# Kernel tuning notes

Measured on AMD Instinct MI355X. Metric: run time of the kernel, lower is better.

## Reference

```python
import jax, jax.numpy as jnp
import numpy as np

S = 4  # HMM states
# allowed transitions among the 4 recurrent states (plus self-loops);
# the (0,4) edge targets a terminal state outside the recurrent block and is omitted
_allow = np.zeros((S, S), dtype=bool)
for i, j in [(0, 0), (1, 1), (2, 2), (3, 3), (0, 1), (1, 2), (2, 3), (0, 2), (1, 3)]:
    _allow[i, j] = True
MASK = jnp.asarray(_allow)
NEG = -1e9


def setup_inputs() -> dict:
    key = jax.random.key(0)
    k0, k1, k2, k3, k4 = jax.random.split(key, 5)
    return {
        "x": jax.random.normal(k0, (256, 4096, 26), dtype=jnp.float32),
        "emit_logits": jax.random.normal(k1, (S, 26), dtype=jnp.float32) * 0.3,
        "trans_logits": jax.random.normal(k2, (S, S), dtype=jnp.float32) * 0.3,
        "init_logits": jax.random.normal(k3, (S,), dtype=jnp.float32) * 0.3,
        "w_out": jax.random.normal(k4, (1, S, 5), dtype=jnp.float32) * 0.3,
    }


def _posterior(x, emit_logits, trans_logits, init_logits):
    # x: [B,T,A] logits -> softmax over alphabet (as in call())
    p = jax.nn.softmax(x, axis=-1)                       # [B,T,A]
    Bmat = jax.nn.softmax(emit_logits, axis=-1)          # [S,A] emission distributions
    # expected emission likelihood per state, in log space
    log_emit = jnp.log(jnp.einsum('bta,sa->bts', p, Bmat) + 1e-16)  # [B,T,S]

    neg = jnp.asarray(NEG, x.dtype)
    logA = jax.nn.log_softmax(jnp.where(MASK, trans_logits, neg), axis=-1)
    logA = jnp.where(MASK, logA, neg)                    # [S,S]
    log_pi = jax.nn.log_softmax(init_logits)             # [S]

    le = jnp.moveaxis(log_emit, 1, 0)                    # [T,B,S]
    T = le.shape[0]

    # forward recursion: alpha_t = e_t + LSE_prev(alpha_{t-1} + logA)
    a0 = log_pi[None, :] + le[0]                         # [B,S]
    def fstep(carry, e):
        nc = e + jax.nn.logsumexp(carry[:, :, None] + logA[None], axis=1)
        return nc, nc
    _, alphas = jax.lax.scan(fstep, a0, le[1:])
    alphas = jnp.concatenate([a0[None], alphas], axis=0)  # [T,B,S]

    # backward recursion: beta_t = LSE_next(logA + e_{t+1} + beta_{t+1})
    bT = jnp.zeros_like(a0)
    def bstep(carry, e_next):
        nc = jax.nn.logsumexp(logA[None] + (e_next + carry)[:, None, :], axis=2)
        return nc, nc
    _, betas = jax.lax.scan(bstep, bT, le[1:], reverse=True)
    betas = jnp.concatenate([betas, bT[None]], axis=0)    # [T,B,S]

    gamma = jax.nn.softmax(alphas + betas, axis=-1)       # posterior [T,B,S]
    return jnp.moveaxis(gamma, 0, 1)[:, :, None, :]       # [B,T,1,S]


def reference(x, emit_logits, trans_logits, init_logits, w_out):
    gamma = _posterior(x, emit_logits, trans_logits, init_logits)  # [B,T,1,S]
    return jnp.einsum('bthd,hdo->bto', gamma, w_out)               # [B,T,5]
```

## Files before the change

### kernel.cpp

```cpp
#include <hip/hip_runtime.h>

#define TDIM 4096
#define BDIM 256
#define ADIM 26
#define SDIM 4
#define NEGF -1e30f
#define LOG2E 1.44269504088896340736f

__device__ __forceinline__ float ex2(float x) { return __builtin_amdgcn_exp2f(x); }
__device__ __forceinline__ float lg2(float x) { return __builtin_amdgcn_logf(x); }

__device__ __forceinline__ float l2se2(float a, float b) {
    float mx = fmaxf(a, b), mn = fminf(a, b);
    return mx + lg2(1.f + ex2(mn - mx));
}
__device__ __forceinline__ float l2se3(float a, float b, float c) {
    float mx = fmaxf(fmaxf(a, b), c);
    float md = __builtin_amdgcn_fmed3f(a, b, c);
    float mn = fminf(fminf(a, b), c);
    return mx + lg2(1.f + ex2(md - mx) + ex2(mn - mx));
}
__device__ __forceinline__ float l2se4(float a, float b, float c, float d) {
    float h1 = fmaxf(a, b), l1 = fminf(a, b);
    float h2 = fmaxf(c, d), l2 = fminf(c, d);
    float mx = fmaxf(h1, h2), s2 = fminf(h1, h2);
    return mx + lg2(1.f + ex2(s2 - mx) + ex2(l1 - mx) + ex2(l2 - mx));
}

struct TransA { float A00, A01, A02, A11, A12, A13, A22, A23, A33; };

__device__ __forceinline__ TransA make_transA(const float* __restrict__ trans) {
    TransA A;
    {
        float l0 = trans[0], l1 = trans[1], l2 = trans[2];
        float m = fmaxf(fmaxf(l0, l1), l2);
        float lz = m + __logf(__expf(l0 - m) + __expf(l1 - m) + __expf(l2 - m));
        A.A00 = (l0 - lz) * LOG2E; A.A01 = (l1 - lz) * LOG2E; A.A02 = (l2 - lz) * LOG2E;
    }
    {
        float l1 = trans[5], l2 = trans[6], l3 = trans[7];
        float m = fmaxf(fmaxf(l1, l2), l3);
        float lz = m + __logf(__expf(l1 - m) + __expf(l2 - m) + __expf(l3 - m));
        A.A11 = (l1 - lz) * LOG2E; A.A12 = (l2 - lz) * LOG2E; A.A13 = (l3 - lz) * LOG2E;
    }
    {
        float l2 = trans[10], l3 = trans[11];
        float m = fmaxf(l2, l3);
        float lz = m + __logf(__expf(l2 - m) + __expf(l3 - m));
        A.A22 = (l2 - lz) * LOG2E; A.A23 = (l3 - lz) * LOG2E;
    }
    A.A33 = 0.f;
    return A;
}

struct UT { float m00, m01, m02, m03, m11, m12, m13, m22, m23, m33; };

__device__ __forceinline__ void fstep(UT& M, const TransA& A, float4 e) {
    float n00 = M.m00 + A.A00 + e.x;
    float n01 = l2se2(M.m00 + A.A01, M.m01 + A.A11) + e.y;
    float n02 = l2se3(M.m00 + A.A02, M.m01 + A.A12, M.m02 + A.A22) + e.z;
    float n03 = l2se3(M.m01 + A.A13, M.m02 + A.A23, M.m03) + e.w;
    float n11 = M.m11 + A.A11 + e.y;
    float n12 = l2se2(M.m11 + A.A12, M.m12 + A.A22) + e.z;
    float n13 = l2se3(M.m11 + A.A13, M.m12 + A.A23, M.m13) + e.w;
    float n22 = M.m22 + A.A22 + e.z;
    float n23 = l2se2(M.m22 + A.A23, M.m23) + e.w;
    float n33 = M.m33 + e.w;
    M.m00 = n00; M.m01 = n01; M.m02 = n02; M.m03 = n03;
    M.m11 = n11; M.m12 = n12; M.m13 = n13; M.m22 = n22; M.m23 = n23; M.m33 = n33;
}

__device__ __forceinline__ UT ut_compose(const UT& A, const UT& B) {
    UT C;
    C.m00 = A.m00 + B.m00;
    C.m01 = l2se2(A.m00 + B.m01, A.m01 + B.m11);
    C.m02 = l2se3(A.m00 + B.m02, A.m01 + B.m12, A.m02 + B.m22);
    C.m03 = l2se4(A.m00 + B.m03, A.m01 + B.m13, A.m02 + B.m23, A.m03 + B.m33);
    C.m11 = A.m11 + B.m11;
    C.m12 = l2se2(A.m11 + B.m12, A.m12 + B.m22);
    C.m13 = l2se3(A.m11 + B.m13, A.m12 + B.m23, A.m13 + B.m33);
    C.m22 = A.m22 + B.m22;
    C.m23 = l2se2(A.m22 + B.m23, A.m23 + B.m33);
    C.m33 = A.m33 + B.m33;
    return C;
}

__device__ __forceinline__ void ut_renorm(UT& M) {
    float m1 = fmaxf(fmaxf(M.m00, M.m01), fmaxf(M.m02, M.m03));
    float m2 = fmaxf(fmaxf(M.m11, M.m12), fmaxf(M.m13, M.m22));
    float m3 = fmaxf(M.m23, M.m33);
    float mx = fmaxf(fmaxf(m1, m2), m3);
    M.m00 -= mx; M.m01 -= mx; M.m02 -= mx; M.m03 -= mx;
    M.m11 -= mx; M.m12 -= mx; M.m13 -= mx; M.m22 -= mx; M.m23 -= mx; M.m33 -= mx;
}

__device__ __forceinline__ void ut_store11(float* p, const UT& M) {
    p[0] = M.m00; p[1] = M.m01; p[2] = M.m02; p[3] = M.m03;
    p[4] = M.m11; p[5] = M.m12; p[6] = M.m13;
    p[7] = M.m22; p[8] = M.m23; p[9] = M.m33;
}
__device__ __forceinline__ UT ut_load11(const float* p) {
    UT M;
    M.m00 = p[0]; M.m01 = p[1]; M.m02 = p[2]; M.m03 = p[3];
    M.m11 = p[4]; M.m12 = p[5]; M.m13 = p[6];
    M.m22 = p[7]; M.m23 = p[8]; M.m33 = p[9];
    return M;
}

__device__ __forceinline__ void vecmat(float& v0, float& v1, float& v2, float& v3,
                                       const float* m) {
    float n0 = v0 + m[0];
    float n1 = l2se2(v0 + m[1], v1 + m[4]);
    float n2 = l2se3(v0 + m[2], v1 + m[5], v2 + m[7]);
    float n3 = l2se4(v0 + m[3], v1 + m[6], v2 + m[8], v3 + m[9]);
    float mm = fmaxf(fmaxf(n0, n1), fmaxf(n2, n3));
    v0 = n0 - mm; v1 = n1 - mm; v2 = n2 - mm; v3 = n3 - mm;
}
__device__ __forceinline__ void matvec(const float* m,
                                       float& u0, float& u1, float& u2, float& u3) {
    float n0 = l2se4(m[0] + u0, m[1] + u1, m[2] + u2, m[3] + u3);
    float n1 = l2se3(m[4] + u1, m[5] + u2, m[6] + u3);
    float n2 = l2se2(m[7] + u2, m[8] + u3);
    float n3 = m[9] + u3;
    float mm = fmaxf(fmaxf(n0, n1), fmaxf(n2, n3));
    u0 = n0 - mm; u1 = n1 - mm; u2 = n2 - mm; u3 = n3 - mm;
}

#define ASTEP(E) do { \
    float4 _e = (E); \
    float n0_ = a0 + A.A00; \
    float n1_ = l2se2(a0 + A.A01, a1 + A.A11); \
    float n2_ = l2se3(a0 + A.A02, a1 + A.A12, a2 + A.A22); \
    float n3_ = l2se3(a1 + A.A13, a2 + A.A23, a3); \
    a0 = n0_ + _e.x; a1 = n1_ + _e.y; a2 = n2_ + _e.z; a3 = n3_ + _e.w; \
    float mm_ = fmaxf(fmaxf(a0, a1), fmaxf(a2, a3)); \
    a0 -= mm_; a1 -= mm_; a2 -= mm_; a3 -= mm_; \
} while (0)

#define BSTEP(E) do { \
    float4 _e = (E); \
    float f0_ = _e.x + b0, f1_ = _e.y + b1, f2_ = _e.z + b2, f3_ = _e.w + b3; \
    float n0_ = l2se3(A.A00 + f0_, A.A01 + f1_, A.A02 + f2_); \
    float n1_ = l2se3(A.A11 + f1_, A.A12 + f2_, A.A13 + f3_); \
    float n2_ = l2se2(A.A22 + f2_, A.A23 + f3_); \
    float n3_ = f3_; \
    float bm_ = fmaxf(fmaxf(n0_, n1_), fmaxf(n2_, n3_)); \
    b0 = n0_ - bm_; b1 = n1_ - bm_; b2 = n2_ - bm_; b3 = n3_ - bm_; \
} while (0)

#define GEMIT(AV, Q) do { \
    float g0_ = (AV).x + b0, g1_ = (AV).y + b1, g2_ = (AV).z + b2, g3_ = (AV).w + b3; \
    float gm_ = fmaxf(fmaxf(g0_, g1_), fmaxf(g2_, g3_)); \
    float q0_ = ex2(g0_ - gm_), q1_ = ex2(g1_ - gm_); \
    float q2_ = ex2(g2_ - gm_), q3_ = ex2(g3_ - gm_); \
    float inv_ = 1.f / (q0_ + q1_ + q2_ + q3_); \
    q0_ *= inv_; q1_ *= inv_; q2_ *= inv_; q3_ *= inv_; \
    vals[(Q)*5 + 0] = fmaf(q0_, wv[0][0], fmaf(q1_, wv[1][0], fmaf(q2_, wv[2][0], q3_ * wv[3][0]))); \
    vals[(Q)*5 + 1] = fmaf(q0_, wv[0][1], fmaf(q1_, wv[1][1], fmaf(q2_, wv[2][1], q3_ * wv[3][1]))); \
    vals[(Q)*5 + 2] = fmaf(q0_, wv[0][2], fmaf(q1_, wv[1][2], fmaf(q2_, wv[2][2], q3_ * wv[3][2]))); \
    vals[(Q)*5 + 3] = fmaf(q0_, wv[0][3], fmaf(q1_, wv[1][3], fmaf(q2_, wv[2][3], q3_ * wv[3][3]))); \
    vals[(Q)*5 + 4] = fmaf(q0_, wv[0][4], fmaf(q1_, wv[1][4], fmaf(q2_, wv[2][4], q3_ * wv[3][4]))); \
} while (0)

#define RDLE(T) sle[(((T) & 15) * 257) + ((T) >> 4)]

#define L0F 0
#define L0B 2816
#define L1F 5632
#define L1B 7040
#define L2F 8448
#define L2B 9152
#define L3F 9856
#define L3B 10208
#define SF  10560
#define SB  10688

__global__ __launch_bounds__(512, 1)
void fused_kernel(const float* __restrict__ x, const float* __restrict__ emit,
                  const float* __restrict__ trans, const float* __restrict__ initl,
                  const float* __restrict__ w, float* __restrict__ out) {
    __shared__ float4 sle[16 * 257];
    __shared__ float4 uni[4096];
    __shared__ float Bmat[SDIM][ADIM];

    float* U = reinterpret_cast<float*>(uni);
    float4* abuf = uni;
    float4* bbuf = uni + 2048;

    const int tid = threadIdx.x;
    const int bidb = blockIdx.x;

    if (tid < SDIM) {
        float m = -1e30f;
        #pragma unroll
        for (int a = 0; a < ADIM; ++a) m = fmaxf(m, emit[tid * ADIM + a]);
        float tmp[ADIM];
        float z = 0.f;
        #pragma unroll
        for (int a = 0; a < ADIM; ++a) {
            float e = __expf(emit[tid * ADIM + a] - m);
            tmp[a] = e; z += e;
        }
        float inv = 1.f / z;
        #pragma unroll
        for (int a = 0; a < ADIM; ++a) Bmat[tid][a] = tmp[a] * inv;
    }
    TransA A = make_transA(trans);
    __syncthreads();

    {
        const float4* xbase = reinterpret_cast<const float4*>(x) + (size_t)bidb * 2048 * 13;
        #pragma unroll 1
        for (int i = 0; i < 4; ++i) {
            const float4* xp = xbase + ((size_t)(i * 512 + tid)) * 13;
            float4 buf[13];
            #pragma unroll
            for (int q = 0; q < 13; ++q) buf[q] = xp[q];

            float d00 = 0.f, d01 = 0.f, d02 = 0.f, d03 = 0.f;
            float d10 = 0.f, d11 = 0.f, d12 = 0.f, d13 = 0.f;
            #pragma unroll
            for (int q = 0; q < 13; ++q) {
                float4 u = buf[q];
                #pragma unroll
                for (int j = 0; j < 4; ++j) {
                    const int e = q * 4 + j;
                    float val = (j == 0) ? u.x : (j == 1) ? u.y : (j == 2) ? u.z : u.w;
                    float ev = ex2(val * LOG2E);
                    if (e < ADIM) {
                        d00 = fmaf(ev, Bmat[0][e], d00); d01 = fmaf(ev, Bmat[1][e], d01);
                        d02 = fmaf(ev, Bmat[2][e], d02); d03 = fmaf(ev, Bmat[3][e], d03);
                    } else {
                        const int a = e - ADIM;
                        d10 = fmaf(ev, Bmat[0][a], d10); d11 = fmaf(ev, Bmat[1][a], d11);
                        d12 = fmaf(ev, Bmat[2][a], d12); d13 = fmaf(ev, Bmat[3][a], d13);
                    }
                }
            }
            float4 r0, r1;
            r0.x = lg2(d00); r0.y = lg2(d01); r0.z = lg2(d02); r0.w = lg2(d03);
            r1.x = lg2(d10); r1.y = lg2(d11); r1.z = lg2(d12); r1.w = lg2(d13);
            int t = (i * 512 + tid) << 1;
            RDLE(t) = r0;
            RDLE(t + 1) = r1;
        }
    }
    __syncthreads();

    const int c = tid & 255;
    const int t0 = c * 16;
    const bool isB = tid >= 256;

    {
        UT M;
        if (!isB) {
            float4 e0 = RDLE(t0);
            if (c == 0) {
                M.m00 = e0.x; M.m11 = e0.y; M.m22 = e0.z; M.m33 = e0.w;
                M.m01 = NEGF; M.m02 = NEGF; M.m03 = NEGF; M.m12 = NEGF; M.m13 = NEGF; M.m23 = NEGF;
            } else {
                M.m00 = A.A00 + e0.x; M.m01 = A.A01 + e0.y; M.m02 = A.A02 + e0.z; M.m03 = NEGF;
                M.m11 = A.A11 + e0.y; M.m12 = A.A12 + e0.z; M.m13 = A.A13 + e0.w;
                M.m22 = A.A22 + e0.z; M.m23 = A.A23 + e0.w; M.m33 = e0.w;
            }
            #pragma unroll 1
            for (int k = 1; k < 16; ++k) fstep(M, A, RDLE(t0 + k));
            ut_renorm(M);
            ut_store11(U + L0F + c * 11, M);
        } else {
            M.m00 = 0.f; M.m11 = 0.f; M.m22 = 0.f; M.m33 = 0.f;
            M.m01 = NEGF; M.m02 = NEGF; M.m03 = NEGF; M.m12 = NEGF; M.m13 = NEGF; M.m23 = NEGF;
            int nst = (c == 255) ? 15 : 16;
            #pragma unroll 1
            for (int k = 0; k < nst; ++k) fstep(M, A, RDLE(t0 + 1 + k));
            ut_renorm(M);
            ut_store11(U + L0B + c * 11, M);
        }
    }
    __syncthreads();

    if (tid < 256) {
        int dir = tid >> 7;
        int i = tid & 127;
        const float* src = U + (dir ? L0B : L0F);
        float* dst = U + (dir ? L1B : L1F);
        UT P = ut_compose(ut_load11(src + (2 * i) * 11), ut_load11(src + (2 * i + 1) * 11));
        ut_renorm(P);
        ut_store11(dst + i * 11, P);
    }
    __syncthreads();

    if (tid < 128) {
        int dir = tid >> 6;
        int i = tid & 63;
        const float* src = U + (dir ? L1B : L1F);
        float* dst = U + (dir ? L2B : L2F);
        UT P = ut_compose(ut_load11(src + (2 * i) * 11), ut_load11(src + (2 * i + 1) * 11));
        ut_renorm(P);
        ut_store11(dst + i * 11, P);
    }
    __syncthreads();

    if (tid < 64) {
        int dir = tid >> 5;
        int i = tid & 31;
        const float* src = U + (dir ? L2B : L2F);
        float* dst = U + (dir ? L3B : L3F);
        UT P = ut_compose(ut_load11(src + (2 * i) * 11), ut_load11(src + (2 * i + 1) * 11));
        ut_renorm(P);
        ut_store11(dst + i * 11, P);
    }
    __syncthreads();

    if (tid == 0) {
        float i0 = initl[0], i1 = initl[1], i2 = initl[2], i3 = initl[3];
        float m = fmaxf(fmaxf(i0, i1), fmaxf(i2, i3));
        float lz = m + __logf(__expf(i0 - m) + __expf(i1 - m) + __expf(i2 - m) + __expf(i3 - m));
        float v0 = (i0 - lz) * LOG2E, v1 = (i1 - lz) * LOG2E;
        float v2 = (i2 - lz) * LOG2E, v3 = (i3 - lz) * LOG2E;
        #pragma unroll 1
        for (int g = 0; g < 32; ++g) {
            U[SF + g * 4 + 0] = v0; U[SF + g * 4 + 1] = v1;
            U[SF + g * 4 + 2] = v2; U[SF + g * 4 + 3] = v3;
            vecmat(v0, v1, v2, v3, U + L3F + g * 11);
        }
    } else if (tid == 64) {
        float u0 = 0.f, u1 = 0.f, u2 = 0.f, u3 = 0.f;
        #pragma unroll 1
        for (int g = 31; g >= 0; --g) {
            U[SB + g * 4 + 0] = u0; U[SB + g * 4 + 1] = u1;
            U[SB + g * 4 + 2] = u2; U[SB + g * 4 + 3] = u3;
            matvec(U + L3B + g * 11, u0, u1, u2, u3);
        }
    }
    __syncthreads();

    float fa0, fa1, fa2, fa3;
    float fb0, fb1, fb2, fb3;
    {
        int g = c >> 3;
        if (!isB) {
            fa0 = U[SF + g * 4 + 0]; fa1 = U[SF + g * 4 + 1];
            fa2 = U[SF + g * 4 + 2]; fa3 = U[SF + g * 4 + 3];
            if (c & 4) vecmat(fa0, fa1, fa2, fa3, U + L2F + (2 * g) * 11);
            if (c & 2) vecmat(fa0, fa1, fa2, fa3, U + L1F + ((c >> 2) * 2) * 11);
            if (c & 1) vecmat(fa0, fa1, fa2, fa3, U + L0F + (c - 1) * 11);
        } else {
            fb0 = U[SB + g * 4 + 0]; fb1 = U[SB + g * 4 + 1];
            fb2 = U[SB + g * 4 + 2]; fb3 = U[SB + g * 4 + 3];
            if (!(c & 4)) matvec(U + L2B + (2 * g + 1) * 11, fb0, fb1, fb2, fb3);
            if (!(c & 2)) matvec(U + L1B + ((c >> 2) * 2 + 1) * 11, fb0, fb1, fb2, fb3);
            if (!(c & 1)) matvec(U + L0B + (c + 1) * 11, fb0, fb1, fb2, fb3);
        }
    }
    __syncthreads();

    float wv[SDIM][5];
    #pragma unroll
    for (int s = 0; s < SDIM; ++s)
        #pragma unroll
        for (int o = 0; o < 5; ++o) wv[s][o] = w[s * 5 + o];

    float* opb = out + (size_t)bidb * TDIM * 5;
    float vals[20];

    if (!isB) {
        float a0 = fa0, a1 = fa1, a2 = fa2, a3 = fa3;
        if (c == 0) {
            float4 e = RDLE(0);
            a0 += e.x; a1 += e.y; a2 += e.z; a3 += e.w;
            float mm = fmaxf(fmaxf(a0, a1), fmaxf(a2, a3));
            a0 -= mm; a1 -= mm; a2 -= mm; a3 -= mm;
        } else {
            ASTEP(RDLE(t0));
        }
        abuf[0 * 256 + c] = make_float4(a0, a1, a2, a3);
        #pragma unroll 1
        for (int k = 1; k < 8; ++k) {
            ASTEP(RDLE(t0 + k));
            abuf[k * 256 + c] = make_float4(a0, a1, a2, a3);
        }
        __syncthreads();
        float b0, b1, b2, b3;
        #pragma unroll 1
        for (int g2 = 0; g2 < 2; ++g2) {
            #pragma unroll
            for (int q = 0; q < 4; ++q) {
                int k = 8 + g2 * 4 + q;
                ASTEP(RDLE(t0 + k));
                float4 bv = bbuf[(k - 8) * 256 + c];
                b0 = bv.x; b1 = bv.y; b2 = bv.z; b3 = bv.w;
                float4 av = make_float4(a0, a1, a2, a3);
                GEMIT(av, q);
            }
            float4* vo = reinterpret_cast<float4*>(opb + (size_t)(t0 + 8 + g2 * 4) * 5);
            vo[0] = make_float4(vals[0],  vals[1],  vals[2],  vals[3]);
            vo[1] = make_float4(vals[4],  vals[5],  vals[6],  vals[7]);
            vo[2] = make_float4(vals[8],  vals[9],  vals[10], vals[11]);
            vo[3] = make_float4(vals[12], vals[13], vals[14], vals[15]);
            vo[4] = make_float4(vals[16], vals[17], vals[18], vals[19]);
        }
    } else {
        float b0 = fb0, b1 = fb1, b2 = fb2, b3 = fb3;
        bool lastc = (c == 255);
        #pragma unroll 1
        for (int k = 15; k >= 8; --k) {
            if (!(lastc && k == 15)) BSTEP(RDLE(t0 + 1 + k));
            bbuf[(k - 8) * 256 + c] = make_float4(b0, b1, b2, b3);
        }
        __syncthreads();
        #pragma unroll 1
        for (int g2 = 1; g2 >= 0; --g2) {
            #pragma unroll
            for (int q = 3; q >= 0; --q) {
                int k = g2 * 4 + q;
                BSTEP(RDLE(t0 + 1 + k));
                float4 av = abuf[k * 256 + c];
                GEMIT(av, q);
            }
            float4* vo = reinterpret_cast<float4*>(opb + (size_t)(t0 + g2 * 4) * 5);
            vo[0] = make_float4(vals[0],  vals[1],  vals[2],  vals[3]);
            vo[1] = make_float4(vals[4],  vals[5],  vals[6],  vals[7]);
            vo[2] = make_float4(vals[8],  vals[9],  vals[10], vals[11]);
            vo[3] = make_float4(vals[12], vals[13], vals[14], vals[15]);
            vo[4] = make_float4(vals[16], vals[17], vals[18], vals[19]);
        }
    }
}

extern "C" void kernel_launch(void* const* d_in, const int* in_sizes, int n_in,
                              void* d_out, int out_size, void* d_ws, size_t ws_size,
                              hipStream_t stream) {
    const float* x     = (const float*)d_in[0];
    const float* emit  = (const float*)d_in[1];
    const float* trans = (const float*)d_in[2];
    const float* initl = (const float*)d_in[3];
    const float* w     = (const float*)d_in[4];
    float* out = (float*)d_out;

    hipLaunchKernelGGL(fused_kernel, dim3(BDIM), dim3(512), 0, stream,
                       x, emit, trans, initl, w, out);
}
```

Measured before the change: 47.50 us.

## Double threads per block and halve chunk length in parallel-scan HMM

Raises the block from 512 to 1024 threads so each forward/backward thread handles 8 timesteps instead of 16. An extra level is added to the composition tree of transition matrices, and the shared-memory layouts and offsets are resized to match. The aim is to shorten the serial per-thread chain and hide more latency with more waves per CU. In exchange there is one more tree level and barrier, more shared memory, and more registers per thread count limit under launch_bounds 1024.

```diff
diff --git a/kernel.cpp b/kernel.cpp
--- a/kernel.cpp
+++ b/kernel.cpp
@@ -162,25 +162,27 @@
     vals[(Q)*5 + 4] = fmaf(q0_, wv[0][4], fmaf(q1_, wv[1][4], fmaf(q2_, wv[2][4], q3_ * wv[3][4]))); \
 } while (0)
 
-#define RDLE(T) sle[(((T) & 15) * 257) + ((T) >> 4)]
+#define RDLE(T) sle[(((T) & 7) * 513) + ((T) >> 3)]
 
 #define L0F 0
-#define L0B 2816
-#define L1F 5632
-#define L1B 7040
-#define L2F 8448
-#define L2B 9152
-#define L3F 9856
-#define L3B 10208
-#define SF  10560
-#define SB  10688
-
-__global__ __launch_bounds__(512, 1)
+#define L0B 5632
+#define L1F 11264
+#define L1B 14080
+#define L2F 16896
+#define L2B 18304
+#define L3F 19712
+#define L3B 20416
+#define L4F 21120
+#define L4B 21472
+#define SF  21824
+#define SB  21952
+
+__global__ __launch_bounds__(1024, 1)
 void fused_kernel(const float* __restrict__ x, const float* __restrict__ emit,
                   const float* __restrict__ trans, const float* __restrict__ initl,
                   const float* __restrict__ w, float* __restrict__ out) {
-    __shared__ float4 sle[16 * 257];
-    __shared__ float4 uni[4096];
+    __shared__ float4 sle[8 * 513];
+    __shared__ float4 uni[5520];
     __shared__ float Bmat[SDIM][ADIM];
 
     float* U = reinterpret_cast<float*>(uni);
@@ -211,8 +213,8 @@
     {
         const float4* xbase = reinterpret_cast<const float4*>(x) + (size_t)bidb * 2048 * 13;
         #pragma unroll 1
-        for (int i = 0; i < 4; ++i) {
-            const float4* xp = xbase + ((size_t)(i * 512 + tid)) * 13;
+        for (int i = 0; i < 2; ++i) {
+            const float4* xp = xbase + ((size_t)(i * 1024 + tid)) * 13;
             float4 buf[13];
             #pragma unroll
             for (int q = 0; q < 13; ++q) buf[q] = xp[q];
@@ -240,16 +242,16 @@
             float4 r0, r1;
             r0.x = lg2(d00); r0.y = lg2(d01); r0.z = lg2(d02); r0.w = lg2(d03);
             r1.x = lg2(d10); r1.y = lg2(d11); r1.z = lg2(d12); r1.w = lg2(d13);
-            int t = (i * 512 + tid) << 1;
+            int t = (i * 1024 + tid) << 1;
             RDLE(t) = r0;
             RDLE(t + 1) = r1;
         }
     }
     __syncthreads();
 
-    const int c = tid & 255;
-    const int t0 = c * 16;
-    const bool isB = tid >= 256;
+    const int c = tid & 511;
+    const int t0 = c * 8;
+    const bool isB = tid >= 512;
 
     {
         UT M;
@@ -264,13 +266,13 @@
                 M.m22 = A.A22 + e0.z; M.m23 = A.A23 + e0.w; M.m33 = e0.w;
             }
             #pragma unroll 1
-            for (int k = 1; k < 16; ++k) fstep(M, A, RDLE(t0 + k));
+            for (int k = 1; k < 8; ++k) fstep(M, A, RDLE(t0 + k));
             ut_renorm(M);
             ut_store11(U + L0F + c * 11, M);
         } else {
             M.m00 = 0.f; M.m11 = 0.f; M.m22 = 0.f; M.m33 = 0.f;
             M.m01 = NEGF; M.m02 = NEGF; M.m03 = NEGF; M.m12 = NEGF; M.m13 = NEGF; M.m23 = NEGF;
-            int nst = (c == 255) ? 15 : 16;
+            int nst = (c == 511) ? 7 : 8;
             #pragma unroll 1
             for (int k = 0; k < nst; ++k) fstep(M, A, RDLE(t0 + 1 + k));
             ut_renorm(M);
@@ -279,9 +281,8 @@
     }
     __syncthreads();
 
-    if (tid < 256) {
-        int dir = tid >> 7;
-        int i = tid & 127;
+    if (tid < 512) {
+        int dir = tid >> 8, i = tid & 255;
         const float* src = U + (dir ? L0B : L0F);
         float* dst = U + (dir ? L1B : L1F);
         UT P = ut_compose(ut_load11(src + (2 * i) * 11), ut_load11(src + (2 * i + 1) * 11));
@@ -290,9 +291,8 @@
     }
     __syncthreads();
 
-    if (tid < 128) {
-        int dir = tid >> 6;
-        int i = tid & 63;
+    if (tid < 256) {
+        int dir = tid >> 7, i = tid & 127;
         const float* src = U + (dir ? L1B : L1F);
         float* dst = U + (dir ? L2B : L2F);
         UT P = ut_compose(ut_load11(src + (2 * i) * 11), ut_load11(src + (2 * i + 1) * 11));
@@ -301,11 +301,20 @@
     }
     __syncthreads();
 
-    if (tid < 64) {
-        int dir = tid >> 5;
-        int i = tid & 31;
+    if (tid < 128) {
+        int dir = tid >> 6, i = tid & 63;
         const float* src = U + (dir ? L2B : L2F);
         float* dst = U + (dir ? L3B : L3F);
+        UT P = ut_compose(ut_load11(src + (2 * i) * 11), ut_load11(src + (2 * i + 1) * 11));
+        ut_renorm(P);
+        ut_store11(dst + i * 11, P);
+    }
+    __syncthreads();
+
+    if (tid < 64) {
+        int dir = tid >> 5, i = tid & 31;
+        const float* src = U + (dir ? L3B : L3F);
+        float* dst = U + (dir ? L4B : L4F);
         UT P = ut_compose(ut_load11(src + (2 * i) * 11), ut_load11(src + (2 * i + 1) * 11));
         ut_renorm(P);
         ut_store11(dst + i * 11, P);
@@ -322,7 +331,7 @@
         for (int g = 0; g < 32; ++g) {
             U[SF + g * 4 + 0] = v0; U[SF + g * 4 + 1] = v1;
             U[SF + g * 4 + 2] = v2; U[SF + g * 4 + 3] = v3;
-            vecmat(v0, v1, v2, v3, U + L3F + g * 11);
+            vecmat(v0, v1, v2, v3, U + L4F + g * 11);
         }
     } else if (tid == 64) {
         float u0 = 0.f, u1 = 0.f, u2 = 0.f, u3 = 0.f;
@@ -330,7 +339,7 @@
         for (int g = 31; g >= 0; --g) {
             U[SB + g * 4 + 0] = u0; U[SB + g * 4 + 1] = u1;
             U[SB + g * 4 + 2] = u2; U[SB + g * 4 + 3] = u3;
-            matvec(U + L3B + g * 11, u0, u1, u2, u3);
+            matvec(U + L4B + g * 11, u0, u1, u2, u3);
         }
     }
     __syncthreads();
@@ -338,17 +347,19 @@
     float fa0, fa1, fa2, fa3;
     float fb0, fb1, fb2, fb3;
     {
-        int g = c >> 3;
+        int g = c >> 4;
         if (!isB) {
             fa0 = U[SF + g * 4 + 0]; fa1 = U[SF + g * 4 + 1];
             fa2 = U[SF + g * 4 + 2]; fa3 = U[SF + g * 4 + 3];
-            if (c & 4) vecmat(fa0, fa1, fa2, fa3, U + L2F + (2 * g) * 11);
+            if (c & 8) vecmat(fa0, fa1, fa2, fa3, U + L3F + (2 * g) * 11);
+            if (c & 4) vecmat(fa0, fa1, fa2, fa3, U + L2F + ((c >> 3) * 2) * 11);
             if (c & 2) vecmat(fa0, fa1, fa2, fa3, U + L1F + ((c >> 2) * 2) * 11);
             if (c & 1) vecmat(fa0, fa1, fa2, fa3, U + L0F + (c - 1) * 11);
         } else {
             fb0 = U[SB + g * 4 + 0]; fb1 = U[SB + g * 4 + 1];
             fb2 = U[SB + g * 4 + 2]; fb3 = U[SB + g * 4 + 3];
-            if (!(c & 4)) matvec(U + L2B + (2 * g + 1) * 11, fb0, fb1, fb2, fb3);
+            if (!(c & 8)) matvec(U + L3B + (2 * g + 1) * 11, fb0, fb1, fb2, fb3);
+            if (!(c & 4)) matvec(U + L2B + ((c >> 3) * 2 + 1) * 11, fb0, fb1, fb2, fb3);
             if (!(c & 2)) matvec(U + L1B + ((c >> 2) * 2 + 1) * 11, fb0, fb1, fb2, fb3);
             if (!(c & 1)) matvec(U + L0B + (c + 1) * 11, fb0, fb1, fb2, fb3);
         }
@@ -374,57 +385,50 @@
         } else {
             ASTEP(RDLE(t0));
         }
-        abuf[0 * 256 + c] = make_float4(a0, a1, a2, a3);
+        abuf[0 * 512 + c] = make_float4(a0, a1, a2, a3);
         #pragma unroll 1
-        for (int k = 1; k < 8; ++k) {
+        for (int k = 1; k < 4; ++k) {
             ASTEP(RDLE(t0 + k));
-            abuf[k * 256 + c] = make_float4(a0, a1, a2, a3);
+            abuf[k * 512 + c] = make_float4(a0, a1, a2, a3);
         }
         __syncthreads();
         float b0, b1, b2, b3;
-        #pragma unroll 1
-        for (int g2 = 0; g2 < 2; ++g2) {
-            #pragma unroll
-            for (int q = 0; q < 4; ++q) {
-                int k = 8 + g2 * 4 + q;
-                ASTEP(RDLE(t0 + k));
-                float4 bv = bbuf[(k - 8) * 256 + c];
-                b0 = bv.x; b1 = bv.y; b2 = bv.z; b3 = bv.w;
-                float4 av = make_float4(a0, a1, a2, a3);
-                GEMIT(av, q);
-            }
-            float4* vo = reinterpret_cast<float4*>(opb + (size_t)(t0 + 8 + g2 * 4) * 5);
-            vo[0] = make_float4(vals[0],  vals[1],  vals[2],  vals[3]);
-            vo[1] = make_float4(vals[4],  vals[5],  vals[6],  vals[7]);
-            vo[2] = make_float4(vals[8],  vals[9],  vals[10], vals[11]);
-            vo[3] = make_float4(vals[12], vals[13], vals[14], vals[15]);
-            vo[4] = make_float4(vals[16], vals[17], vals[18], vals[19]);
-        }
+        #pragma unroll
+        for (int q = 0; q < 4; ++q) {
+            int k = 4 + q;
+            ASTEP(RDLE(t0 + k));
+            float4 bv = bbuf[q * 512 + c];
+            b0 = bv.x; b1 = bv.y; b2 = bv.z; b3 = bv.w;
+            float4 av = make_float4(a0, a1, a2, a3);
+            GEMIT(av, q);
+        }
+        float4* vo = reinterpret_cast<float4*>(opb + (size_t)(t0 + 4) * 5);
+        vo[0] = make_float4(vals[0],  vals[1],  vals[2],  vals[3]);
+        vo[1] = make_float4(vals[4],  vals[5],  vals[6],  vals[7]);
+        vo[2] = make_float4(vals[8],  vals[9],  vals[10], vals[11]);
+        vo[3] = make_float4(vals[12], vals[13], vals[14], vals[15]);
+        vo[4] = make_float4(vals[16], vals[17], vals[18], vals[19]);
     } else {
         float b0 = fb0, b1 = fb1, b2 = fb2, b3 = fb3;
-        bool lastc = (c == 255);
+        bool lastc = (c == 511);
         #pragma unroll 1
-        for (int k = 15; k >= 8; --k) {
-            if (!(lastc && k == 15)) BSTEP(RDLE(t0 + 1 + k));
-            bbuf[(k - 8) * 256 + c] = make_float4(b0, b1, b2, b3);
+        for (int k = 7; k >= 4; --k) {
+            if (!(lastc && k == 7)) BSTEP(RDLE(t0 + 1 + k));
+            bbuf[(k - 4) * 512 + c] = make_float4(b0, b1, b2, b3);
         }
         __syncthreads();
-        #pragma unroll 1
-        for (int g2 = 1; g2 >= 0; --g2) {
-            #pragma unroll
-            for (int q = 3; q >= 0; --q) {
-                int k = g2 * 4 + q;
-                BSTEP(RDLE(t0 + 1 + k));
-                float4 av = abuf[k * 256 + c];
-                GEMIT(av, q);
-            }
-            float4* vo = reinterpret_cast<float4*>(opb + (size_t)(t0 + g2 * 4) * 5);
-            vo[0] = make_float4(vals[0],  vals[1],  vals[2],  vals[3]);
-            vo[1] = make_float4(vals[4],  vals[5],  vals[6],  vals[7]);
-            vo[2] = make_float4(vals[8],  vals[9],  vals[10], vals[11]);
-            vo[3] = make_float4(vals[12], vals[13], vals[14], vals[15]);
-            vo[4] = make_float4(vals[16], vals[17], vals[18], vals[19]);
-        }
+        #pragma unroll
+        for (int q = 3; q >= 0; --q) {
+            BSTEP(RDLE(t0 + 1 + q));
+            float4 av = abuf[q * 512 + c];
+            GEMIT(av, q);
+        }
+        float4* vo = reinterpret_cast<float4*>(opb + (size_t)t0 * 5);
+        vo[0] = make_float4(vals[0],  vals[1],  vals[2],  vals[3]);
+        vo[1] = make_float4(vals[4],  vals[5],  vals[6],  vals[7]);
+        vo[2] = make_float4(vals[8],  vals[9],  vals[10], vals[11]);
+        vo[3] = make_float4(vals[12], vals[13], vals[14], vals[15]);
+        vo[4] = make_float4(vals[16], vals[17], vals[18], vals[19]);
     }
 }
 
@@ -438,6 +442,6 @@
     const float* w     = (const float*)d_in[4];
     float* out = (float*)d_out;
 
-    hipLaunchKernelGGL(fused_kernel, dim3(BDIM), dim3(512), 0, stream,
+    hipLaunchKernelGGL(fused_kernel, dim3(BDIM), dim3(1024), 0, stream,
                        x, emit, trans, initl, w, out);
 }
```

Measured after the change: 112.1 us. +136.0%, slower.

## Switch forward-backward recursion from log-space to scaled linear-space arithmetic

Applied to the files above, without the earlier changes.

Replaces all log-sum-exp semiring operations (forward/backward steps, matrix composition, vecmat/matvec, posterior) with ordinary multiply-add in probability space, renormalising by the max via a hardware reciprocal each step. This removes many exp2/log2 transcendental calls per step and the log of emission likelihoods, leaving mostly FMAs. In exchange it relies on per-step rescaling to avoid underflow, and products of up to 16 steps before renorm in fstep are rescaled each step, so precision risk is modest; rcp approximation adds small error.

```diff
diff --git a/kernel.cpp b/kernel.cpp
--- a/kernel.cpp
+++ b/kernel.cpp
@@ -4,28 +4,10 @@
 #define BDIM 256
 #define ADIM 26
 #define SDIM 4
-#define NEGF -1e30f
 #define LOG2E 1.44269504088896340736f
 
 __device__ __forceinline__ float ex2(float x) { return __builtin_amdgcn_exp2f(x); }
-__device__ __forceinline__ float lg2(float x) { return __builtin_amdgcn_logf(x); }
-
-__device__ __forceinline__ float l2se2(float a, float b) {
-    float mx = fmaxf(a, b), mn = fminf(a, b);
-    return mx + lg2(1.f + ex2(mn - mx));
-}
-__device__ __forceinline__ float l2se3(float a, float b, float c) {
-    float mx = fmaxf(fmaxf(a, b), c);
-    float md = __builtin_amdgcn_fmed3f(a, b, c);
-    float mn = fminf(fminf(a, b), c);
-    return mx + lg2(1.f + ex2(md - mx) + ex2(mn - mx));
-}
-__device__ __forceinline__ float l2se4(float a, float b, float c, float d) {
-    float h1 = fmaxf(a, b), l1 = fminf(a, b);
-    float h2 = fmaxf(c, d), l2 = fminf(c, d);
-    float mx = fmaxf(h1, h2), s2 = fminf(h1, h2);
-    return mx + lg2(1.f + ex2(s2 - mx) + ex2(l1 - mx) + ex2(l2 - mx));
-}
+__device__ __forceinline__ float rcp(float x) { return __builtin_amdgcn_rcpf(x); }
 
 struct TransA { float A00, A01, A02, A11, A12, A13, A22, A23, A33; };
 
@@ -34,64 +16,70 @@
     {
         float l0 = trans[0], l1 = trans[1], l2 = trans[2];
         float m = fmaxf(fmaxf(l0, l1), l2);
-        float lz = m + __logf(__expf(l0 - m) + __expf(l1 - m) + __expf(l2 - m));
-        A.A00 = (l0 - lz) * LOG2E; A.A01 = (l1 - lz) * LOG2E; A.A02 = (l2 - lz) * LOG2E;
+        float e0 = __expf(l0 - m), e1 = __expf(l1 - m), e2 = __expf(l2 - m);
+        float s = 1.f / (e0 + e1 + e2);
+        A.A00 = e0 * s; A.A01 = e1 * s; A.A02 = e2 * s;
     }
     {
         float l1 = trans[5], l2 = trans[6], l3 = trans[7];
         float m = fmaxf(fmaxf(l1, l2), l3);
-        float lz = m + __logf(__expf(l1 - m) + __expf(l2 - m) + __expf(l3 - m));
-        A.A11 = (l1 - lz) * LOG2E; A.A12 = (l2 - lz) * LOG2E; A.A13 = (l3 - lz) * LOG2E;
+        float e1 = __expf(l1 - m), e2 = __expf(l2 - m), e3 = __expf(l3 - m);
+        float s = 1.f / (e1 + e2 + e3);
+        A.A11 = e1 * s; A.A12 = e2 * s; A.A13 = e3 * s;
     }
     {
         float l2 = trans[10], l3 = trans[11];
         float m = fmaxf(l2, l3);
-        float lz = m + __logf(__expf(l2 - m) + __expf(l3 - m));
-        A.A22 = (l2 - lz) * LOG2E; A.A23 = (l3 - lz) * LOG2E;
-    }
-    A.A33 = 0.f;
+        float e2 = __expf(l2 - m), e3 = __expf(l3 - m);
+        float s = 1.f / (e2 + e3);
+        A.A22 = e2 * s; A.A23 = e3 * s;
+    }
+    A.A33 = 1.f;
     return A;
 }
 
 struct UT { float m00, m01, m02, m03, m11, m12, m13, m22, m23, m33; };
 
 __device__ __forceinline__ void fstep(UT& M, const TransA& A, float4 e) {
-    float n00 = M.m00 + A.A00 + e.x;
-    float n01 = l2se2(M.m00 + A.A01, M.m01 + A.A11) + e.y;
-    float n02 = l2se3(M.m00 + A.A02, M.m01 + A.A12, M.m02 + A.A22) + e.z;
-    float n03 = l2se3(M.m01 + A.A13, M.m02 + A.A23, M.m03) + e.w;
-    float n11 = M.m11 + A.A11 + e.y;
-    float n12 = l2se2(M.m11 + A.A12, M.m12 + A.A22) + e.z;
-    float n13 = l2se3(M.m11 + A.A13, M.m12 + A.A23, M.m13) + e.w;
-    float n22 = M.m22 + A.A22 + e.z;
-    float n23 = l2se2(M.m22 + A.A23, M.m23) + e.w;
-    float n33 = M.m33 + e.w;
-    M.m00 = n00; M.m01 = n01; M.m02 = n02; M.m03 = n03;
-    M.m11 = n11; M.m12 = n12; M.m13 = n13; M.m22 = n22; M.m23 = n23; M.m33 = n33;
+    float n00 = M.m00 * A.A00 * e.x;
+    float n01 = fmaf(M.m00, A.A01, M.m01 * A.A11) * e.y;
+    float n02 = fmaf(M.m00, A.A02, fmaf(M.m01, A.A12, M.m02 * A.A22)) * e.z;
+    float n03 = fmaf(M.m01, A.A13, fmaf(M.m02, A.A23, M.m03)) * e.w;
+    float n11 = M.m11 * A.A11 * e.y;
+    float n12 = fmaf(M.m11, A.A12, M.m12 * A.A22) * e.z;
+    float n13 = fmaf(M.m11, A.A13, fmaf(M.m12, A.A23, M.m13)) * e.w;
+    float n22 = M.m22 * A.A22 * e.z;
+    float n23 = fmaf(M.m22, A.A23, M.m23) * e.w;
+    float n33 = M.m33 * e.w;
+    float m1 = fmaxf(fmaxf(n00, n01), fmaxf(n02, n03));
+    float m2 = fmaxf(fmaxf(n11, n12), fmaxf(n13, n22));
+    float s = rcp(fmaxf(fmaxf(m1, m2), fmaxf(n23, n33)));
+    M.m00 = n00 * s; M.m01 = n01 * s; M.m02 = n02 * s; M.m03 = n03 * s;
+    M.m11 = n11 * s; M.m12 = n12 * s; M.m13 = n13 * s;
+    M.m22 = n22 * s; M.m23 = n23 * s; M.m33 = n33 * s;
 }
 
 __device__ __forceinline__ UT ut_compose(const UT& A, const UT& B) {
     UT C;
-    C.m00 = A.m00 + B.m00;
-    C.m01 = l2se2(A.m00 + B.m01, A.m01 + B.m11);
-    C.m02 = l2se3(A.m00 + B.m02, A.m01 + B.m12, A.m02 + B.m22);
-    C.m03 = l2se4(A.m00 + B.m03, A.m01 + B.m13, A.m02 + B.m23, A.m03 + B.m33);
-    C.m11 = A.m11 + B.m11;
-    C.m12 = l2se2(A.m11 + B.m12, A.m12 + B.m22);
-    C.m13 = l2se3(A.m11 + B.m13, A.m12 + B.m23, A.m13 + B.m33);
-    C.m22 = A.m22 + B.m22;
-    C.m23 = l2se2(A.m22 + B.m23, A.m23 + B.m33);
-    C.m33 = A.m33 + B.m33;
+    C.m00 = A.m00 * B.m00;
+    C.m01 = fmaf(A.m00, B.m01, A.m01 * B.m11);
+    C.m02 = fmaf(A.m00, B.m02, fmaf(A.m01, B.m12, A.m02 * B.m22));
+    C.m03 = fmaf(A.m00, B.m03, fmaf(A.m01, B.m13, fmaf(A.m02, B.m23, A.m03 * B.m33)));
+    C.m11 = A.m11 * B.m11;
+    C.m12 = fmaf(A.m11, B.m12, A.m12 * B.m22);
+    C.m13 = fmaf(A.m11, B.m13, fmaf(A.m12, B.m23, A.m13 * B.m33));
+    C.m22 = A.m22 * B.m22;
+    C.m23 = fmaf(A.m22, B.m23, A.m23 * B.m33);
+    C.m33 = A.m33 * B.m33;
     return C;
 }
 
 __device__ __forceinline__ void ut_renorm(UT& M) {
     float m1 = fmaxf(fmaxf(M.m00, M.m01), fmaxf(M.m02, M.m03));
     float m2 = fmaxf(fmaxf(M.m11, M.m12), fmaxf(M.m13, M.m22));
-    float m3 = fmaxf(M.m23, M.m33);
-    float mx = fmaxf(fmaxf(m1, m2), m3);
-    M.m00 -= mx; M.m01 -= mx; M.m02 -= mx; M.m03 -= mx;
-    M.m11 -= mx; M.m12 -= mx; M.m13 -= mx; M.m22 -= mx; M.m23 -= mx; M.m33 -= mx;
+    float s = rcp(fmaxf(fmaxf(m1, m2), fmaxf(M.m23, M.m33)));
+    M.m00 *= s; M.m01 *= s; M.m02 *= s; M.m03 *= s;
+    M.m11 *= s; M.m12 *= s; M.m13 *= s; M.m22 *= s; M.m23 *= s; M.m33 *= s;
 }
 
 __device__ __forceinline__ void ut_store11(float* p, const UT& M) {
@@ -109,52 +97,48 @@
 
 __device__ __forceinline__ void vecmat(float& v0, float& v1, float& v2, float& v3,
                                        const float* m) {
-    float n0 = v0 + m[0];
-    float n1 = l2se2(v0 + m[1], v1 + m[4]);
-    float n2 = l2se3(v0 + m[2], v1 + m[5], v2 + m[7]);
-    float n3 = l2se4(v0 + m[3], v1 + m[6], v2 + m[8], v3 + m[9]);
-    float mm = fmaxf(fmaxf(n0, n1), fmaxf(n2, n3));
-    v0 = n0 - mm; v1 = n1 - mm; v2 = n2 - mm; v3 = n3 - mm;
+    float n0 = v0 * m[0];
+    float n1 = fmaf(v0, m[1], v1 * m[4]);
+    float n2 = fmaf(v0, m[2], fmaf(v1, m[5], v2 * m[7]));
+    float n3 = fmaf(v0, m[3], fmaf(v1, m[6], fmaf(v2, m[8], v3 * m[9])));
+    float s = rcp(fmaxf(fmaxf(n0, n1), fmaxf(n2, n3)));
+    v0 = n0 * s; v1 = n1 * s; v2 = n2 * s; v3 = n3 * s;
 }
 __device__ __forceinline__ void matvec(const float* m,
                                        float& u0, float& u1, float& u2, float& u3) {
-    float n0 = l2se4(m[0] + u0, m[1] + u1, m[2] + u2, m[3] + u3);
-    float n1 = l2se3(m[4] + u1, m[5] + u2, m[6] + u3);
-    float n2 = l2se2(m[7] + u2, m[8] + u3);
-    float n3 = m[9] + u3;
-    float mm = fmaxf(fmaxf(n0, n1), fmaxf(n2, n3));
-    u0 = n0 - mm; u1 = n1 - mm; u2 = n2 - mm; u3 = n3 - mm;
+    float n0 = fmaf(m[0], u0, fmaf(m[1], u1, fmaf(m[2], u2, m[3] * u3)));
+    float n1 = fmaf(m[4], u1, fmaf(m[5], u2, m[6] * u3));
+    float n2 = fmaf(m[7], u2, m[8] * u3);
+    float n3 = m[9] * u3;
+    float s = rcp(fmaxf(fmaxf(n0, n1), fmaxf(n2, n3)));
+    u0 = n0 * s; u1 = n1 * s; u2 = n2 * s; u3 = n3 * s;
 }
 
 #define ASTEP(E) do { \
     float4 _e = (E); \
-    float n0_ = a0 + A.A00; \
-    float n1_ = l2se2(a0 + A.A01, a1 + A.A11); \
-    float n2_ = l2se3(a0 + A.A02, a1 + A.A12, a2 + A.A22); \
-    float n3_ = l2se3(a1 + A.A13, a2 + A.A23, a3); \
-    a0 = n0_ + _e.x; a1 = n1_ + _e.y; a2 = n2_ + _e.z; a3 = n3_ + _e.w; \
-    float mm_ = fmaxf(fmaxf(a0, a1), fmaxf(a2, a3)); \
-    a0 -= mm_; a1 -= mm_; a2 -= mm_; a3 -= mm_; \
+    float n0_ = a0 * A.A00 * _e.x; \
+    float n1_ = fmaf(a0, A.A01, a1 * A.A11) * _e.y; \
+    float n2_ = fmaf(a0, A.A02, fmaf(a1, A.A12, a2 * A.A22)) * _e.z; \
+    float n3_ = fmaf(a1, A.A13, fmaf(a2, A.A23, a3)) * _e.w; \
+    float s_ = rcp(fmaxf(fmaxf(n0_, n1_), fmaxf(n2_, n3_))); \
+    a0 = n0_ * s_; a1 = n1_ * s_; a2 = n2_ * s_; a3 = n3_ * s_; \
 } while (0)
 
 #define BSTEP(E) do { \
     float4 _e = (E); \
-    float f0_ = _e.x + b0, f1_ = _e.y + b1, f2_ = _e.z + b2, f3_ = _e.w + b3; \
-    float n0_ = l2se3(A.A00 + f0_, A.A01 + f1_, A.A02 + f2_); \
-    float n1_ = l2se3(A.A11 + f1_, A.A12 + f2_, A.A13 + f3_); \
-    float n2_ = l2se2(A.A22 + f2_, A.A23 + f3_); \
+    float f0_ = _e.x * b0, f1_ = _e.y * b1, f2_ = _e.z * b2, f3_ = _e.w * b3; \
+    float n0_ = fmaf(A.A00, f0_, fmaf(A.A01, f1_, A.A02 * f2_)); \
+    float n1_ = fmaf(A.A11, f1_, fmaf(A.A12, f2_, A.A13 * f3_)); \
+    float n2_ = fmaf(A.A22, f2_, A.A23 * f3_); \
     float n3_ = f3_; \
-    float bm_ = fmaxf(fmaxf(n0_, n1_), fmaxf(n2_, n3_)); \
-    b0 = n0_ - bm_; b1 = n1_ - bm_; b2 = n2_ - bm_; b3 = n3_ - bm_; \
+    float s_ = rcp(fmaxf(fmaxf(n0_, n1_), fmaxf(n2_, n3_))); \
+    b0 = n0_ * s_; b1 = n1_ * s_; b2 = n2_ * s_; b3 = n3_ * s_; \
 } while (0)
 
 #define GEMIT(AV, Q) do { \
-    float g0_ = (AV).x + b0, g1_ = (AV).y + b1, g2_ = (AV).z + b2, g3_ = (AV).w + b3; \
-    float gm_ = fmaxf(fmaxf(g0_, g1_), fmaxf(g2_, g3_)); \
-    float q0_ = ex2(g0_ - gm_), q1_ = ex2(g1_ - gm_); \
-    float q2_ = ex2(g2_ - gm_), q3_ = ex2(g3_ - gm_); \
-    float inv_ = 1.f / (q0_ + q1_ + q2_ + q3_); \
-    q0_ *= inv_; q1_ *= inv_; q2_ *= inv_; q3_ *= inv_; \
+    float g0_ = (AV).x * b0, g1_ = (AV).y * b1, g2_ = (AV).z * b2, g3_ = (AV).w * b3; \
+    float inv_ = rcp(g0_ + g1_ + g2_ + g3_); \
+    float q0_ = g0_ * inv_, q1_ = g1_ * inv_, q2_ = g2_ * inv_, q3_ = g3_ * inv_; \
     vals[(Q)*5 + 0] = fmaf(q0_, wv[0][0], fmaf(q1_, wv[1][0], fmaf(q2_, wv[2][0], q3_ * wv[3][0]))); \
     vals[(Q)*5 + 1] = fmaf(q0_, wv[0][1], fmaf(q1_, wv[1][1], fmaf(q2_, wv[2][1], q3_ * wv[3][1]))); \
     vals[(Q)*5 + 2] = fmaf(q0_, wv[0][2], fmaf(q1_, wv[1][2], fmaf(q2_, wv[2][2], q3_ * wv[3][2]))); \
@@ -237,12 +221,9 @@
                     }
                 }
             }
-            float4 r0, r1;
-            r0.x = lg2(d00); r0.y = lg2(d01); r0.z = lg2(d02); r0.w = lg2(d03);
-            r1.x = lg2(d10); r1.y = lg2(d11); r1.z = lg2(d12); r1.w = lg2(d13);
             int t = (i * 512 + tid) << 1;
-            RDLE(t) = r0;
-            RDLE(t + 1) = r1;
+            RDLE(t) = make_float4(d00, d01, d02, d03);
+            RDLE(t + 1) = make_float4(d10, d11, d12, d13);
         }
     }
     __syncthreads();
@@ -257,19 +238,19 @@
             float4 e0 = RDLE(t0);
             if (c == 0) {
                 M.m00 = e0.x; M.m11 = e0.y; M.m22 = e0.z; M.m33 = e0.w;
-                M.m01 = NEGF; M.m02 = NEGF; M.m03 = NEGF; M.m12 = NEGF; M.m13 = NEGF; M.m23 = NEGF;
+                M.m01 = 0.f; M.m02 = 0.f; M.m03 = 0.f; M.m12 = 0.f; M.m13 = 0.f; M.m23 = 0.f;
             } else {
-                M.m00 = A.A00 + e0.x; M.m01 = A.A01 + e0.y; M.m02 = A.A02 + e0.z; M.m03 = NEGF;
-                M.m11 = A.A11 + e0.y; M.m12 = A.A12 + e0.z; M.m13 = A.A13 + e0.w;
-                M.m22 = A.A22 + e0.z; M.m23 = A.A23 + e0.w; M.m33 = e0.w;
+                M.m00 = A.A00 * e0.x; M.m01 = A.A01 * e0.y; M.m02 = A.A02 * e0.z; M.m03 = 0.f;
+                M.m11 = A.A11 * e0.y; M.m12 = A.A12 * e0.z; M.m13 = A.A13 * e0.w;
+                M.m22 = A.A22 * e0.z; M.m23 = A.A23 * e0.w; M.m33 = e0.w;
             }
             #pragma unroll 1
             for (int k = 1; k < 16; ++k) fstep(M, A, RDLE(t0 + k));
             ut_renorm(M);
             ut_store11(U + L0F + c * 11, M);
         } else {
-            M.m00 = 0.f; M.m11 = 0.f; M.m22 = 0.f; M.m33 = 0.f;
-            M.m01 = NEGF; M.m02 = NEGF; M.m03 = NEGF; M.m12 = NEGF; M.m13 = NEGF; M.m23 = NEGF;
+            M.m00 = 1.f; M.m11 = 1.f; M.m22 = 1.f; M.m33 = 1.f;
+            M.m01 = 0.f; M.m02 = 0.f; M.m03 = 0.f; M.m12 = 0.f; M.m13 = 0.f; M.m23 = 0.f;
             int nst = (c == 255) ? 15 : 16;
             #pragma unroll 1
             for (int k = 0; k < nst; ++k) fstep(M, A, RDLE(t0 + 1 + k));
@@ -315,9 +296,9 @@
     if (tid == 0) {
         float i0 = initl[0], i1 = initl[1], i2 = initl[2], i3 = initl[3];
         float m = fmaxf(fmaxf(i0, i1), fmaxf(i2, i3));
-        float lz = m + __logf(__expf(i0 - m) + __expf(i1 - m) + __expf(i2 - m) + __expf(i3 - m));
-        float v0 = (i0 - lz) * LOG2E, v1 = (i1 - lz) * LOG2E;
-        float v2 = (i2 - lz) * LOG2E, v3 = (i3 - lz) * LOG2E;
+        float e0 = __expf(i0 - m), e1 = __expf(i1 - m), e2 = __expf(i2 - m), e3 = __expf(i3 - m);
+        float s = 1.f / (e0 + e1 + e2 + e3);
+        float v0 = e0 * s, v1 = e1 * s, v2 = e2 * s, v3 = e3 * s;
         #pragma unroll 1
         for (int g = 0; g < 32; ++g) {
             U[SF + g * 4 + 0] = v0; U[SF + g * 4 + 1] = v1;
@@ -325,7 +306,7 @@
             vecmat(v0, v1, v2, v3, U + L3F + g * 11);
         }
     } else if (tid == 64) {
-        float u0 = 0.f, u1 = 0.f, u2 = 0.f, u3 = 0.f;
+        float u0 = 1.f, u1 = 1.f, u2 = 1.f, u3 = 1.f;
         #pragma unroll 1
         for (int g = 31; g >= 0; --g) {
             U[SB + g * 4 + 0] = u0; U[SB + g * 4 + 1] = u1;
@@ -368,9 +349,9 @@
         float a0 = fa0, a1 = fa1, a2 = fa2, a3 = fa3;
         if (c == 0) {
             float4 e = RDLE(0);
-            a0 += e.x; a1 += e.y; a2 += e.z; a3 += e.w;
-            float mm = fmaxf(fmaxf(a0, a1), fmaxf(a2, a3));
-            a0 -= mm; a1 -= mm; a2 -= mm; a3 -= mm;
+            float n0 = a0 * e.x, n1 = a1 * e.y, n2 = a2 * e.z, n3 = a3 * e.w;
+            float s = rcp(fmaxf(fmaxf(n0, n1), fmaxf(n2, n3)));
+            a0 = n0 * s; a1 = n1 * s; a2 = n2 * s; a3 = n3 * s;
         } else {
             ASTEP(RDLE(t0));
         }
```

Result: faster. 40.38 us (-15.0%).
